# Kernel tuning notes

Measured on AMD Instinct MI355X. Metric: run time of the kernel, lower is better.

## Reference

```python
import jax, jax.numpy as jnp
import numpy as np

N, C, HW, HEADS = 2048, 16, 8, 4
F = C * HW * HW  # 1024
E = 16384
EPS = 1e-5
NEG_SLOPE = 0.2


def _bn(x, g, b):
    # training-mode BatchNorm2d over (N, H, W)
    m = x.mean(axis=(0, 2, 3), keepdims=True)
    v = x.var(axis=(0, 2, 3), keepdims=True)
    return (x - m) * jax.lax.rsqrt(v + EPS) * g[None, :, None, None] + b[None, :, None, None]


def _conv1x1(x, w, b):
    # 1x1 conv == per-pixel linear: w is [out_c, in_c]
    return jnp.einsum('nchw,oc->nohw', x, w) + b[None, :, None, None]


def _gatv2(xf, edge_index, wl, bl, wr, br, att, bias_gat):
    # xf: [N, F] node features
    xl = (xf @ wl + bl).reshape(N, HEADS, F)  # source-side transform (lin_l)
    xr = (xf @ wr + br).reshape(N, HEADS, F)  # target-side transform (lin_r)
    src, dst = edge_index[0], edge_index[1]
    loops = jnp.arange(N)
    # PyG default: remove existing self loops (mask them) then add self loops
    src_f = jnp.concatenate([src, loops])
    dst_f = jnp.concatenate([dst, loops])
    valid = jnp.concatenate([src != dst, jnp.ones((N,), bool)])
    xj = xl[src_f]                                   # [E+N, HEADS, F] gather
    e = jax.nn.leaky_relu(xj + xr[dst_f], negative_slope=NEG_SLOPE)
    logits = jnp.einsum('ehf,hf->eh', e, att)        # [E+N, HEADS]
    logits = jnp.where(valid[:, None], logits, -jnp.inf)
    mx = jax.lax.stop_gradient(jax.ops.segment_max(logits, dst_f, num_segments=N))
    expv = jnp.where(valid[:, None], jnp.exp(logits - mx[dst_f]), 0.0)
    denom = jax.ops.segment_sum(expv, dst_f, num_segments=N)
    alpha = expv / denom[dst_f]                      # segment softmax over incoming edges
    out = jax.ops.segment_sum(alpha[:, :, None] * xj, dst_f, num_segments=N)  # [N, HEADS, F]
    return out.reshape(N, HEADS * F) + bias_gat


def setup_inputs() -> dict:
    key = jax.random.key(0)
    ks = jax.random.split(key, 8)
    s = 0.02
    return {
        'x': jax.random.normal(ks[0], (N, C, HW, HW), jnp.float32),
        'edge_index': jax.random.randint(ks[1], (2, E), 0, N),
        'w1': jax.random.normal(ks[2], (C, C), jnp.float32) * s,
        'b1': jnp.zeros((C,), jnp.float32),
        'g1': jnp.ones((C,), jnp.float32),
        'be1': jnp.zeros((C,), jnp.float32),
        'wl': jax.random.normal(ks[3], (F, HEADS * F), jnp.float32) * s,
        'bl': jnp.zeros((HEADS * F,), jnp.float32),
        'wr': jax.random.normal(ks[4], (F, HEADS * F), jnp.float32) * s,
        'br': jnp.zeros((HEADS * F,), jnp.float32),
        'att': jax.random.normal(ks[5], (HEADS, F), jnp.float32) * s,
        'bias_gat': jnp.zeros((HEADS * F,), jnp.float32),
        'w2': jax.random.normal(ks[6], (C, HEADS * C), jnp.float32) * s,
        'b2': jnp.zeros((C,), jnp.float32),
        'g2': jnp.ones((C,), jnp.float32),
        'be2': jnp.zeros((C,), jnp.float32),
    }


def reference(x, edge_index, w1, b1, g1, be1, wl, bl, wr, br, att, bias_gat, w2, b2, g2, be2):
    res = x
    y = _bn(_conv1x1(x, w1, b1), g1, be1)            # fc1: Conv2d 1x1 + BN
    yf = y.reshape(N, F)
    g = _gatv2(yf, edge_index, wl, bl, wr, br, att, bias_gat)
    g = g.reshape(N, HEADS * C, HW, HW)
    out = _bn(_conv1x1(g, w2, b2), g2, be2)          # fc2: Conv2d 1x1 + BN
    return out + res                                  # DropPath(0.0) == Identity
```

## Files before the change

kernel.cpp:

```cpp
#include <hip/hip_runtime.h>
#include <stdint.h>

#define N_NODES 2048
#define F_DIM   1024
#define HEADS   4
#define NF      4096
#define ROW     8192
#define E_EDGES 16384
#define MAXE    (E_EDGES + N_NODES)
#define BN_EPS  1e-5f
#define NSLOPE  0.2f

typedef unsigned short ushort_t;
typedef __attribute__((ext_vector_type(8))) short bf16x8;
typedef __attribute__((ext_vector_type(4))) float f32x4;
typedef __attribute__((ext_vector_type(8))) unsigned short us8;

__device__ __forceinline__ float b2f(unsigned short u) {
    union { unsigned int i; float f; } x; x.i = ((unsigned int)u) << 16; return x.f;
}
__device__ __forceinline__ unsigned short f2b(float f) {
    union { float f; unsigned int i; } x; x.f = f;
    unsigned int r = x.i + 0x7fffu + ((x.i >> 16) & 1u);
    return (unsigned short)(r >> 16);
}
__device__ __forceinline__ ushort_t ld_canon(const void* src, size_t i, int f32) {
    return f32 ? f2b(((const float*)src)[i]) : ((const ushort_t*)src)[i];
}
__device__ __forceinline__ float ld_f(const void* src, size_t i, int f32) {
    return f32 ? ((const float*)src)[i] : b2f(((const ushort_t*)src)[i]);
}

__device__ __forceinline__ int sniff_f32_blk(const ushort_t* xu, int* lds_flag) {
    int t = threadIdx.x;
    if (t < 64) {
        unsigned e = (xu[2 * t] >> 7) & 0xFF;
        unsigned long long m = __ballot(e >= 0x90u);
        if (t == 0) *lds_flag = (__popcll(m) >= 3) ? 1 : 0;
    }
    __syncthreads();
    return *lds_flag;
}
__device__ __forceinline__ int sniff_i64_blk(const int* ei_raw, int* lds_flag) {
    int t = threadIdx.x;
    if (t < 64) {
        unsigned long long m = __ballot(ei_raw[2 * t + 1] != 0);
        if (t == 0) *lds_flag = (m == 0ull) ? 1 : 0;
    }
    __syncthreads();
    return *lds_flag;
}

__global__ __launch_bounds__(256) void k_prep(
    const void* __restrict__ wl, const void* __restrict__ wr,
    const int* __restrict__ ei_raw, const ushort_t* __restrict__ xu,
    ushort_t* __restrict__ wT, int* __restrict__ counts)
{
    __shared__ ushort_t tl[64][65];
    __shared__ int sfl;
    int b = blockIdx.x, t = threadIdx.x;
    if (b < 2048) {
        int f32 = sniff_f32_blk(xu, &sfl);
        int z = b >> 10, rem = b & 1023;
        int bx = (rem & 63) * 64, by = (rem >> 6) * 64;
        const void* in = z ? wr : wl;
        ushort_t* outT = wT + (size_t)z * 4194304ull;
        #pragma unroll
        for (int i = 0; i < 16; ++i) {
            int idx = t + i * 256;
            int r = idx >> 6, c = idx & 63;
            tl[r][c] = ld_canon(in, (size_t)(by + r) * 4096 + bx + c, f32);
        }
        __syncthreads();
        #pragma unroll
        for (int i = 0; i < 16; ++i) {
            int idx = t + i * 256;
            int r = idx >> 6, c = idx & 63;
            outT[(size_t)(bx + r) * 1024 + by + c] = tl[c][r];
        }
    } else {
        int i64 = sniff_i64_blk(ei_raw, &sfl);
        int idx = (b - 2048) * 256 + t;
        if (idx < E_EDGES) {
            int s = i64 ? ei_raw[2 * idx] : ei_raw[idx];
            int d = i64 ? ei_raw[2 * (E_EDGES + idx)] : ei_raw[E_EDGES + idx];
            if (s != d) atomicAdd(&counts[d], 1);
        } else if (idx < MAXE) {
            atomicAdd(&counts[idx - E_EDGES], 1);
        }
    }
}

__global__ __launch_bounds__(256) void k_fc1(
    const void* __restrict__ x, const void* __restrict__ w1, const void* __restrict__ b1,
    ushort_t* __restrict__ y0b, float* __restrict__ ps, float* __restrict__ pq)
{
    __shared__ float xs[1024];
    __shared__ float sw[256];
    __shared__ float sb[16];
    __shared__ int sfl;
    int f32 = sniff_f32_blk((const ushort_t*)x, &sfl);
    int tid = threadIdx.x;
    sw[tid] = ld_f(w1, tid, f32);
    if (tid < 16) sb[tid] = ld_f(b1, tid, f32);
    int wave = tid >> 6, lane = tid & 63;
    float s[4] = {0,0,0,0}, q[4] = {0,0,0,0};
    for (int nn = 0; nn < 8; ++nn) {
        int n = blockIdx.x * 8 + nn;
        __syncthreads();
        #pragma unroll
        for (int i = 0; i < 4; ++i) {
            int idx = tid + i * 256;
            xs[idx] = ld_f(x, (size_t)n * 1024 + idx, f32);
        }
        __syncthreads();
        #pragma unroll
        for (int i = 0; i < 4; ++i) {
            int o = wave * 4 + i;
            float acc = sb[o];
            #pragma unroll
            for (int c = 0; c < 16; ++c) acc += xs[c * 64 + lane] * sw[o * 16 + c];
            y0b[(size_t)n * 1024 + o * 64 + lane] = f2b(acc);
            s[i] += acc; q[i] += acc * acc;
        }
    }
    #pragma unroll
    for (int i = 0; i < 4; ++i)
        for (int mm = 1; mm < 64; mm <<= 1) {
            s[i] += __shfl_xor(s[i], mm);
            q[i] += __shfl_xor(q[i], mm);
        }
    if (lane == 0)
        #pragma unroll
        for (int i = 0; i < 4; ++i) {
            ps[blockIdx.x * 16 + wave * 4 + i] = s[i];
            pq[blockIdx.x * 16 + wave * 4 + i] = q[i];
        }
}

__global__ __launch_bounds__(256) void k_mid(
    const int* __restrict__ ei_raw, const int* __restrict__ counts,
    int* __restrict__ cursor, int* __restrict__ offs, int* __restrict__ esrc,
    const float* __restrict__ ps, const float* __restrict__ pq,
    const void* __restrict__ g1, const void* __restrict__ be1,
    const ushort_t* __restrict__ xu, float* __restrict__ ss)
{
    __shared__ int offl[2048];
    __shared__ int ts[256];
    __shared__ int sfl;
    __shared__ float rs[16][16], rq[16][16];
    int t = threadIdx.x;
    if (blockIdx.x < 72) {
        int i64 = sniff_i64_blk(ei_raw, &sfl);
        int loc[8]; int tot = 0;
        #pragma unroll
        for (int j = 0; j < 8; ++j) { loc[j] = counts[t * 8 + j]; tot += loc[j]; }
        ts[t] = tot; __syncthreads();
        for (int s = 1; s < 256; s <<= 1) {
            int v = (t >= s) ? ts[t - s] : 0;
            __syncthreads();
            ts[t] += v;
            __syncthreads();
        }
        int run = ts[t] - tot;
        #pragma unroll
        for (int j = 0; j < 8; ++j) { offl[t * 8 + j] = run; run += loc[j]; }
        __syncthreads();
        if (blockIdx.x == 0) {
            #pragma unroll
            for (int j = 0; j < 8; ++j) offs[t * 8 + j] = offl[t * 8 + j];
            if (t == 255) offs[2048] = run;
        }
        int idx = blockIdx.x * 256 + t;
        if (idx < E_EDGES) {
            int s = i64 ? ei_raw[2 * idx] : ei_raw[idx];
            int d = i64 ? ei_raw[2 * (E_EDGES + idx)] : ei_raw[E_EDGES + idx];
            if (s != d) esrc[offl[d] + atomicAdd(&cursor[d], 1)] = s;
        } else if (idx < MAXE) {
            int n = idx - E_EDGES;
            esrc[offl[n] + atomicAdd(&cursor[n], 1)] = n;
        }
    } else {
        int f32 = sniff_f32_blk(xu, &sfl);
        int ch = t & 15, seg = t >> 4;
        float s = 0.f, q = 0.f;
        for (int j = 0; j < 16; ++j) {
            int b = seg * 16 + j;
            s += ps[b * 16 + ch]; q += pq[b * 16 + ch];
        }
        rs[seg][ch] = s; rq[seg][ch] = q;
        __syncthreads();
        if (t < 16) {
            float S = 0.f, Q = 0.f;
            #pragma unroll
            for (int g = 0; g < 16; ++g) { S += rs[g][t]; Q += rq[g][t]; }
            const float inv = 1.0f / 131072.0f;
            float mean = S * inv;
            float var  = Q * inv - mean * mean;
            float sc = ld_f(g1, t, f32) * rsqrtf(var + BN_EPS);
            ss[t] = sc;
            ss[16 + t] = ld_f(be1, t, f32) - mean * sc;
        }
    }
}

__global__ __launch_bounds__(256) void k_norm(
    const ushort_t* __restrict__ y0b, const float* __restrict__ ss,
    ushort_t* __restrict__ xf)
{
    __shared__ float scs[16], shs[16];
    int t = threadIdx.x;
    if (t < 16) { scs[t] = ss[t]; shs[t] = ss[16 + t]; }
    __syncthreads();
    size_t base = (size_t)blockIdx.x * 4096 + t * 16;
    int ch = ((int)(base >> 6)) & 15;
    float sc = scs[ch], sh = shs[ch];
    us8 v0 = *(const us8*)(y0b + base), v1 = *(const us8*)(y0b + base + 8);
    us8 o0, o1;
    #pragma unroll
    for (int j = 0; j < 8; ++j) {
        o0[j] = f2b(b2f(v0[j]) * sc + sh);
        o1[j] = f2b(b2f(v1[j]) * sc + sh);
    }
    *(us8*)(xf + base) = o0;
    *(us8*)(xf + base + 8) = o1;
}

__global__ __launch_bounds__(256) void k_gemm(
    const ushort_t* __restrict__ A, const ushort_t* __restrict__ BT,
    const void* __restrict__ blr, const void* __restrict__ brr,
    const ushort_t* __restrict__ xu, ushort_t* __restrict__ out)
{
    __shared__ __align__(16) ushort_t smem[16384];
    ushort_t* As0 = smem;
    ushort_t* As1 = smem + 4096;
    ushort_t* Bs0 = smem + 8192;
    ushort_t* Bs1 = smem + 12288;
    ushort_t* cs  = smem;
    __shared__ int sfl;
    int f32 = sniff_f32_blk(xu, &sfl);
    int tid = threadIdx.x;
    int wv = tid >> 6, ln = tid & 63;
    int m0 = blockIdx.y * 128, n0 = blockIdx.x * 128;
    int wm = (wv >> 1) * 64, wn = (wv & 1) * 64;
    int lr = ln & 15, quad = ln >> 4;

    f32x4 acc[4][4];
    #pragma unroll
    for (int i = 0; i < 4; ++i)
        #pragma unroll
        for (int j = 0; j < 4; ++j) acc[i][j] = (f32x4){0.f, 0.f, 0.f, 0.f};

    for (int k0 = 0; k0 < 1024; k0 += 64) {
        #pragma unroll
        for (int i = 0; i < 2; ++i) {
            int cbase = i * 256 + wv * 64;
            int ci = cbase + ln;
            int m = ci >> 2, kc = ci & 3;
            const ushort_t* ga = A + (size_t)(m0 + m) * 1024 + k0 + kc * 8;
            __builtin_amdgcn_global_load_lds(
                (const __attribute__((address_space(1))) void*)ga,
                (__attribute__((address_space(3))) void*)(&As0[cbase * 8]), 16, 0, 0);
            __builtin_amdgcn_global_load_lds(
                (const __attribute__((address_space(1))) void*)(ga + 32),
                (__attribute__((address_space(3))) void*)(&As1[cbase * 8]), 16, 0, 0);
            const ushort_t* gb = BT + (size_t)(n0 + m) * 1024 + k0 + kc * 8;
            __builtin_amdgcn_global_load_lds(
                (const __attribute__((address_space(1))) void*)gb,
                (__attribute__((address_space(3))) void*)(&Bs0[cbase * 8]), 16, 0, 0);
            __builtin_amdgcn_global_load_lds(
                (const __attribute__((address_space(1))) void*)(gb + 32),
                (__attribute__((address_space(3))) void*)(&Bs1[cbase * 8]), 16, 0, 0);
        }
        __syncthreads();
        #pragma unroll
        for (int p = 0; p < 2; ++p) {
            const ushort_t* Ap = p ? As1 : As0;
            const ushort_t* Bp = p ? Bs1 : Bs0;
            bf16x8 af[4], bfr[4];
            #pragma unroll
            for (int i = 0; i < 4; ++i)
                af[i] = *(const bf16x8*)(&Ap[(wm + i * 16 + lr) * 32 + quad * 8]);
            #pragma unroll
            for (int j = 0; j < 4; ++j)
                bfr[j] = *(const bf16x8*)(&Bp[(wn + j * 16 + lr) * 32 + quad * 8]);
            #pragma unroll
            for (int i = 0; i < 4; ++i)
                #pragma unroll
                for (int j = 0; j < 4; ++j)
                    acc[i][j] = __builtin_amdgcn_mfma_f32_16x16x32_bf16(af[i], bfr[j], acc[i][j], 0, 0, 0);
        }
        __syncthreads();
    }
    float bj[4];
    #pragma unroll
    for (int j = 0; j < 4; ++j) {
        int colg = n0 + wn + j * 16 + lr;
        bj[j] = (colg < 4096) ? ld_f(blr, colg, f32) : ld_f(brr, colg - 4096, f32);
    }
    #pragma unroll
    for (int ph = 0; ph < 2; ++ph) {
        if ((wv >> 1) == ph) {
            #pragma unroll
            for (int i = 0; i < 4; ++i)
                #pragma unroll
                for (int j = 0; j < 4; ++j) {
                    int col = wn + j * 16 + lr;
                    #pragma unroll
                    for (int r = 0; r < 4; ++r)
                        cs[(i * 16 + quad * 4 + r) * 136 + col] = f2b(acc[i][j][r] + bj[j]);
                }
        }
        __syncthreads();
        #pragma unroll
        for (int rr = 0; rr < 4; ++rr) {
            int slot = rr * 256 + tid;
            int row = slot >> 4, seg = slot & 15;
            us8 v = *(const us8*)&cs[row * 136 + seg * 8];
            *(us8*)(out + (size_t)(m0 + ph * 64 + row) * ROW + n0 + seg * 8) = v;
        }
        __syncthreads();
    }
}

__global__ __launch_bounds__(64) void k_gat(
    const ushort_t* __restrict__ xlr,
    const void* __restrict__ att, const void* __restrict__ bg,
    const ushort_t* __restrict__ xu,
    const int* __restrict__ offsets, const int* __restrict__ esrc,
    ushort_t* __restrict__ g)
{
    int bx = blockIdx.x;
    int d = bx >> 2, h = bx & 3;
    int l = threadIdx.x;
    int f32;
    {
        unsigned e = (xu[2 * l] >> 7) & 0xFF;
        unsigned long long m = __ballot(e >= 0x90u);
        f32 = (__popcll(m) >= 3) ? 1 : 0;
    }
    int off = offsets[d], deg = offsets[d + 1] - off;
    size_t hF = (size_t)h * F_DIM + l * 16;

    float xrv[16], attv[16];
    {
        const ushort_t* xp = xlr + ((size_t)d * ROW + NF + hF);
        us8 x0 = *(const us8*)xp, x1 = *(const us8*)(xp + 8);
        #pragma unroll
        for (int j = 0; j < 8; ++j) {
            xrv[j] = b2f(x0[j]); xrv[8 + j] = b2f(x1[j]);
            attv[j]     = ld_f(att, hF + j, f32);
            attv[8 + j] = ld_f(att, hF + 8 + j, f32);
        }
    }
    float acc[16];
    #pragma unroll
    for (int j = 0; j < 16; ++j) acc[j] = 0.f;
    float s_run = 0.f;

    for (int c0 = 0; c0 < deg; c0 += 64) {
        int cnt = min(64, deg - c0);
        int eidx = esrc[off + c0 + (l < cnt ? l : 0)];
        int e = 0;
        for (; e + 3 < cnt; e += 4) {
            int i0 = __shfl(eidx, e),     i1 = __shfl(eidx, e + 1);
            int i2 = __shfl(eidx, e + 2), i3 = __shfl(eidx, e + 3);
            const ushort_t* p0 = xlr + ((size_t)i0 * ROW + hF);
            const ushort_t* p1 = xlr + ((size_t)i1 * ROW + hF);
            const ushort_t* p2 = xlr + ((size_t)i2 * ROW + hF);
            const ushort_t* p3 = xlr + ((size_t)i3 * ROW + hF);
            us8 v0[4], v1[4];
            v0[0] = *(const us8*)p0; v1[0] = *(const us8*)(p0 + 8);
            v0[1] = *(const us8*)p1; v1[1] = *(const us8*)(p1 + 8);
            v0[2] = *(const us8*)p2; v1[2] = *(const us8*)(p2 + 8);
            v0[3] = *(const us8*)p3; v1[3] = *(const us8*)(p3 + 8);
            float tt[4];
            #pragma unroll
            for (int k = 0; k < 4; ++k) {
                float t0 = 0.f;
                #pragma unroll
                for (int j = 0; j < 8; ++j) {
                    float u;
                    u = b2f(v0[k][j]) + xrv[j];     u = u > 0.f ? u : NSLOPE * u; t0 += u * attv[j];
                    u = b2f(v1[k][j]) + xrv[8 + j]; u = u > 0.f ? u : NSLOPE * u; t0 += u * attv[8 + j];
                }
                tt[k] = t0;
            }
            #pragma unroll
            for (int mm = 1; mm < 64; mm <<= 1) {
                tt[0] += __shfl_xor(tt[0], mm);
                tt[1] += __shfl_xor(tt[1], mm);
                tt[2] += __shfl_xor(tt[2], mm);
                tt[3] += __shfl_xor(tt[3], mm);
            }
            float w0 = __expf(tt[0]), w1 = __expf(tt[1]);
            float w2v = __expf(tt[2]), w3 = __expf(tt[3]);
            s_run += w0 + w1 + w2v + w3;
            #pragma unroll
            for (int j = 0; j < 8; ++j) {
                acc[j]     += w0 * b2f(v0[0][j]) + w1 * b2f(v0[1][j])
                            + w2v * b2f(v0[2][j]) + w3 * b2f(v0[3][j]);
                acc[8 + j] += w0 * b2f(v1[0][j]) + w1 * b2f(v1[1][j])
                            + w2v * b2f(v1[2][j]) + w3 * b2f(v1[3][j]);
            }
        }
        for (; e < cnt; ++e) {
            int i0 = __shfl(eidx, e);
            const ushort_t* p = xlr + ((size_t)i0 * ROW + hF);
            us8 a0 = *(const us8*)p, a1 = *(const us8*)(p + 8);
            float t0 = 0.f;
            #pragma unroll
            for (int j = 0; j < 8; ++j) {
                float u;
                u = b2f(a0[j]) + xrv[j];     u = u > 0.f ? u : NSLOPE * u; t0 += u * attv[j];
                u = b2f(a1[j]) + xrv[8 + j]; u = u > 0.f ? u : NSLOPE * u; t0 += u * attv[8 + j];
            }
            #pragma unroll
            for (int mm = 1; mm < 64; mm <<= 1) t0 += __shfl_xor(t0, mm);
            float w0 = __expf(t0);
            s_run += w0;
            #pragma unroll
            for (int j = 0; j < 8; ++j) {
                acc[j]     += w0 * b2f(a0[j]);
                acc[8 + j] += w0 * b2f(a1[j]);
            }
        }
    }
    float inv = 1.0f / s_run;
    ushort_t* gp = g + ((size_t)d * NF + hF);
    us8 outv0, outv1;
    #pragma unroll
    for (int j = 0; j < 8; ++j) {
        outv0[j] = f2b(acc[j] * inv + ld_f(bg, hF + j, f32));
        outv1[j] = f2b(acc[8 + j] * inv + ld_f(bg, hF + 8 + j, f32));
    }
    *(us8*)gp = outv0;
    *(us8*)(gp + 8) = outv1;
}

__global__ __launch_bounds__(256) void k_fc2(
    const ushort_t* __restrict__ g, const void* __restrict__ w2, const void* __restrict__ b2,
    const ushort_t* __restrict__ xu,
    ushort_t* __restrict__ zb, float* __restrict__ ps, float* __restrict__ pq)
{
    __shared__ float gs[4096];
    __shared__ float sw[1024];
    __shared__ float sb[16];
    __shared__ int sfl;
    int f32 = sniff_f32_blk(xu, &sfl);
    int tid = threadIdx.x;
    #pragma unroll
    for (int i = 0; i < 4; ++i) sw[tid + i * 256] = ld_f(w2, tid + i * 256, f32);
    if (tid < 16) sb[tid] = ld_f(b2, tid, f32);
    int wave = tid >> 6, lane = tid & 63;
    float s[4] = {0,0,0,0}, q[4] = {0,0,0,0};
    for (int nn = 0; nn < 8; ++nn) {
        int n = blockIdx.x * 8 + nn;
        __syncthreads();
        {
            const ushort_t* gp = g + (size_t)n * 4096 + tid * 16;
            us8 v0 = *(const us8*)gp, v1 = *(const us8*)(gp + 8);
            #pragma unroll
            for (int j = 0; j < 8; ++j) {
                gs[tid * 16 + j] = b2f(v0[j]);
                gs[tid * 16 + 8 + j] = b2f(v1[j]);
            }
        }
        __syncthreads();
        #pragma unroll
        for (int i = 0; i < 4; ++i) {
            int o = wave * 4 + i;
            float acc = sb[o];
            #pragma unroll
            for (int k = 0; k < 64; ++k) acc += gs[k * 64 + lane] * sw[o * 64 + k];
            zb[(size_t)n * 1024 + o * 64 + lane] = f2b(acc);
            s[i] += acc; q[i] += acc * acc;
        }
    }
    #pragma unroll
    for (int i = 0; i < 4; ++i)
        for (int mm = 1; mm < 64; mm <<= 1) {
            s[i] += __shfl_xor(s[i], mm);
            q[i] += __shfl_xor(q[i], mm);
        }
    if (lane == 0)
        #pragma unroll
        for (int i = 0; i < 4; ++i) {
            ps[blockIdx.x * 16 + wave * 4 + i] = s[i];
            pq[blockIdx.x * 16 + wave * 4 + i] = q[i];
        }
}

__global__ __launch_bounds__(256) void k_out(
    const ushort_t* __restrict__ zb, const void* __restrict__ x,
    const float* __restrict__ ps, const float* __restrict__ pq,
    const void* __restrict__ g2, const void* __restrict__ be2,
    void* __restrict__ out)
{
    __shared__ float red[2][64];
    __shared__ float scs[16], shs[16];
    __shared__ int sfl;
    int f32 = sniff_f32_blk((const ushort_t*)x, &sfl);
    int t = threadIdx.x, lane = t & 63, wv = t >> 6;
    float s = 0.f, q = 0.f;
    #pragma unroll
    for (int i = 0; i < 16; ++i) { s += ps[i * 256 + t]; q += pq[i * 256 + t]; }
    s += __shfl_xor(s, 16); q += __shfl_xor(q, 16);
    s += __shfl_xor(s, 32); q += __shfl_xor(q, 32);
    if (lane < 16) { red[0][wv * 16 + lane] = s; red[1][wv * 16 + lane] = q; }
    __syncthreads();
    if (t < 16) {
        float S = red[0][t] + red[0][16 + t] + red[0][32 + t] + red[0][48 + t];
        float Q = red[1][t] + red[1][16 + t] + red[1][32 + t] + red[1][48 + t];
        const float inv = 1.0f / 131072.0f;
        float mean = S * inv;
        float var  = Q * inv - mean * mean;
        float sc = ld_f(g2, t, f32) * rsqrtf(var + BN_EPS);
        scs[t] = sc;
        shs[t] = ld_f(be2, t, f32) - mean * sc;
    }
    __syncthreads();
    size_t base = (size_t)blockIdx.x * 8192;
    #pragma unroll
    for (int i = 0; i < 32; ++i) {
        size_t k = base + t + i * 256;
        int ch = ((int)k >> 6) & 15;
        float val = b2f(zb[k]) * scs[ch] + shs[ch] + ld_f(x, k, f32);
        if (f32) ((float*)out)[k] = val;
        else     ((ushort_t*)out)[k] = f2b(val);
    }
}

extern "C" void kernel_launch(void* const* d_in, const int* in_sizes, int n_in,
                              void* d_out, int out_size, void* d_ws, size_t ws_size,
                              hipStream_t stream)
{
    const void* x   = d_in[0];
    const void* ei  = d_in[1];
    const void* w1  = d_in[2];
    const void* b1  = d_in[3];
    const void* g1  = d_in[4];
    const void* be1 = d_in[5];
    const void* wl  = d_in[6];
    const void* bl  = d_in[7];
    const void* wr  = d_in[8];
    const void* br  = d_in[9];
    const void* att = d_in[10];
    const void* bg  = d_in[11];
    const void* w2  = d_in[12];
    const void* b2  = d_in[13];
    const void* g2  = d_in[14];
    const void* be2 = d_in[15];
    (void)in_sizes; (void)n_in; (void)out_size; (void)ws_size;

    char* wsb = (char*)d_ws;
    size_t o = 0;
    auto alloc = [&](size_t bytes) -> void* {
        void* p = wsb + o;
        o = (o + bytes + 255) & ~(size_t)255;
        return p;
    };
    float*    ss    = (float*)alloc(32 * 4);
    ushort_t* y0b   = (ushort_t*)alloc(2097152ull * 2);
    ushort_t* xf    = (ushort_t*)alloc(2097152ull * 2);
    ushort_t* zb    = (ushort_t*)alloc(2097152ull * 2);
    ushort_t* wT    = (ushort_t*)alloc(8388608ull * 2);
    ushort_t* gbuf  = wT;
    ushort_t* xlr   = (ushort_t*)alloc(16777216ull * 2);
    float* p1s = (float*)alloc(256 * 16 * 4);
    float* p1q = (float*)alloc(256 * 16 * 4);
    float* p2s = (float*)alloc(256 * 16 * 4);
    float* p2q = (float*)alloc(256 * 16 * 4);
    int* counts = (int*)alloc(2048 * 4);
    int* cursor = (int*)alloc(2048 * 4);
    int* offs   = (int*)alloc(2049 * 4);
    int* esrc   = (int*)alloc(MAXE * 4);

    hipMemsetAsync(counts, 0, 2 * 2048 * 4, stream);
    k_prep<<<2120, 256, 0, stream>>>(wl, wr, (const int*)ei, (const ushort_t*)x, wT, counts);
    k_fc1<<<256, 256, 0, stream>>>(x, w1, b1, y0b, p1s, p1q);
    k_mid<<<73, 256, 0, stream>>>((const int*)ei, counts, cursor, offs, esrc,
                                  p1s, p1q, g1, be1, (const ushort_t*)x, ss);
    k_norm<<<512, 256, 0, stream>>>(y0b, ss, xf);
    k_gemm<<<dim3(64, 16), 256, 0, stream>>>(xf, wT, bl, br, (const ushort_t*)x, xlr);
    k_gat<<<N_NODES * HEADS, 64, 0, stream>>>(xlr, att, bg, (const ushort_t*)x, offs, esrc, gbuf);
    k_fc2<<<256, 256, 0, stream>>>(gbuf, w2, b2, (const ushort_t*)x, zb, p2s, p2q);
    k_out<<<256, 256, 0, stream>>>(zb, x, p2s, p2q, g2, be2, d_out);
}
```

Before: 275.6 us.

## Derive fc1 BN stats from input covariance and fuse normalize into conv

Computes BatchNorm statistics for the first 1x1 conv analytically from per-channel input means and the 16x16 input covariance. This lets the conv, scale and shift be folded into a single kernel that writes the normalized bf16 features directly, so the intermediate y0b buffer and the separate normalize pass go away. The price is a second read of x and a reduction over a larger partial-covariance buffer in a single block. It also remaps GEMM block indices so that blocks on the same XCD share N tiles, aiming for better L2 reuse.

```diff
diff --git a/kernel.cpp b/kernel.cpp
--- a/kernel.cpp
+++ b/kernel.cpp
@@ -91,64 +91,49 @@
     }
 }
 
-__global__ __launch_bounds__(256) void k_fc1(
-    const void* __restrict__ x, const void* __restrict__ w1, const void* __restrict__ b1,
-    ushort_t* __restrict__ y0b, float* __restrict__ ps, float* __restrict__ pq)
-{
-    __shared__ float xs[1024];
-    __shared__ float sw[256];
-    __shared__ float sb[16];
+__global__ __launch_bounds__(256) void k_stats(
+    const void* __restrict__ x, const ushort_t* __restrict__ xu,
+    float* __restrict__ psum, float* __restrict__ pcov)
+{
+    __shared__ float xs[16 * 65];
     __shared__ int sfl;
-    int f32 = sniff_f32_blk((const ushort_t*)x, &sfl);
-    int tid = threadIdx.x;
-    sw[tid] = ld_f(w1, tid, f32);
-    if (tid < 16) sb[tid] = ld_f(b1, tid, f32);
-    int wave = tid >> 6, lane = tid & 63;
-    float s[4] = {0,0,0,0}, q[4] = {0,0,0,0};
+    int f32 = sniff_f32_blk(xu, &sfl);
+    int t = threadIdx.x;
+    int c1 = t >> 4, c2 = t & 15;
+    float cov = 0.f, s = 0.f;
     for (int nn = 0; nn < 8; ++nn) {
         int n = blockIdx.x * 8 + nn;
         __syncthreads();
         #pragma unroll
         for (int i = 0; i < 4; ++i) {
-            int idx = tid + i * 256;
-            xs[idx] = ld_f(x, (size_t)n * 1024 + idx, f32);
-        }
-        __syncthreads();
-        #pragma unroll
-        for (int i = 0; i < 4; ++i) {
-            int o = wave * 4 + i;
-            float acc = sb[o];
-            #pragma unroll
-            for (int c = 0; c < 16; ++c) acc += xs[c * 64 + lane] * sw[o * 16 + c];
-            y0b[(size_t)n * 1024 + o * 64 + lane] = f2b(acc);
-            s[i] += acc; q[i] += acc * acc;
-        }
-    }
-    #pragma unroll
-    for (int i = 0; i < 4; ++i)
-        for (int mm = 1; mm < 64; mm <<= 1) {
-            s[i] += __shfl_xor(s[i], mm);
-            q[i] += __shfl_xor(q[i], mm);
-        }
-    if (lane == 0)
-        #pragma unroll
-        for (int i = 0; i < 4; ++i) {
-            ps[blockIdx.x * 16 + wave * 4 + i] = s[i];
-            pq[blockIdx.x * 16 + wave * 4 + i] = q[i];
-        }
+            int idx = t + i * 256;
+            int c = idx >> 6, p = idx & 63;
+            xs[c * 65 + p] = ld_f(x, (size_t)n * 1024 + idx, f32);
+        }
+        __syncthreads();
+        #pragma unroll
+        for (int p = 0; p < 64; ++p)
+            cov += xs[c1 * 65 + p] * xs[c2 * 65 + p];
+        if (t < 16) {
+            #pragma unroll
+            for (int p = 0; p < 64; ++p) s += xs[t * 65 + p];
+        }
+    }
+    pcov[blockIdx.x * 256 + t] = cov;
+    if (t < 16) psum[blockIdx.x * 16 + t] = s;
 }
 
 __global__ __launch_bounds__(256) void k_mid(
     const int* __restrict__ ei_raw, const int* __restrict__ counts,
     int* __restrict__ cursor, int* __restrict__ offs, int* __restrict__ esrc,
-    const float* __restrict__ ps, const float* __restrict__ pq,
+    const float* __restrict__ psum, const float* __restrict__ pcov,
+    const void* __restrict__ w1, const void* __restrict__ b1,
     const void* __restrict__ g1, const void* __restrict__ be1,
     const ushort_t* __restrict__ xu, float* __restrict__ ss)
 {
     __shared__ int offl[2048];
     __shared__ int ts[256];
     __shared__ int sfl;
-    __shared__ float rs[16][16], rq[16][16];
     int t = threadIdx.x;
     if (blockIdx.x < 72) {
         int i64 = sniff_i64_blk(ei_raw, &sfl);
@@ -181,22 +166,30 @@
             esrc[offl[n] + atomicAdd(&cursor[n], 1)] = n;
         }
     } else {
+        __shared__ float covr[256];
+        __shared__ float mu[16];
+        __shared__ float wsh[256];
         int f32 = sniff_f32_blk(xu, &sfl);
-        int ch = t & 15, seg = t >> 4;
-        float s = 0.f, q = 0.f;
-        for (int j = 0; j < 16; ++j) {
-            int b = seg * 16 + j;
-            s += ps[b * 16 + ch]; q += pq[b * 16 + ch];
-        }
-        rs[seg][ch] = s; rq[seg][ch] = q;
-        __syncthreads();
+        float c = 0.f;
+        for (int b = 0; b < 256; ++b) c += pcov[b * 256 + t];
+        covr[t] = c;
+        wsh[t] = ld_f(w1, t, f32);
         if (t < 16) {
-            float S = 0.f, Q = 0.f;
-            #pragma unroll
-            for (int g = 0; g < 16; ++g) { S += rs[g][t]; Q += rq[g][t]; }
+            float s = 0.f;
+            for (int b = 0; b < 256; ++b) s += psum[b * 16 + t];
+            mu[t] = s * (1.0f / 131072.0f);
+        }
+        __syncthreads();
+        if (t < 16) {
             const float inv = 1.0f / 131072.0f;
-            float mean = S * inv;
-            float var  = Q * inv - mean * mean;
+            float mean = ld_f(b1, t, f32);
+            float var = 0.f;
+            for (int ca = 0; ca < 16; ++ca) {
+                float wa = wsh[t * 16 + ca];
+                mean += wa * mu[ca];
+                for (int cb = 0; cb < 16; ++cb)
+                    var += wa * wsh[t * 16 + cb] * (covr[ca * 16 + cb] * inv - mu[ca] * mu[cb]);
+            }
             float sc = ld_f(g1, t, f32) * rsqrtf(var + BN_EPS);
             ss[t] = sc;
             ss[16 + t] = ld_f(be1, t, f32) - mean * sc;
@@ -204,26 +197,41 @@
     }
 }
 
-__global__ __launch_bounds__(256) void k_norm(
-    const ushort_t* __restrict__ y0b, const float* __restrict__ ss,
-    ushort_t* __restrict__ xf)
-{
+__global__ __launch_bounds__(256) void k_fc1n(
+    const void* __restrict__ x, const void* __restrict__ w1, const void* __restrict__ b1,
+    const float* __restrict__ ss, ushort_t* __restrict__ xf)
+{
+    __shared__ float xs[1024];
+    __shared__ float sw[256];
+    __shared__ float sb[16];
     __shared__ float scs[16], shs[16];
-    int t = threadIdx.x;
-    if (t < 16) { scs[t] = ss[t]; shs[t] = ss[16 + t]; }
+    __shared__ int sfl;
+    int f32 = sniff_f32_blk((const ushort_t*)x, &sfl);
+    int tid = threadIdx.x;
+    float wraw = ld_f(w1, tid, f32);
+    if (tid < 16) { scs[tid] = ss[tid]; shs[tid] = ss[16 + tid]; }
     __syncthreads();
-    size_t base = (size_t)blockIdx.x * 4096 + t * 16;
-    int ch = ((int)(base >> 6)) & 15;
-    float sc = scs[ch], sh = shs[ch];
-    us8 v0 = *(const us8*)(y0b + base), v1 = *(const us8*)(y0b + base + 8);
-    us8 o0, o1;
-    #pragma unroll
-    for (int j = 0; j < 8; ++j) {
-        o0[j] = f2b(b2f(v0[j]) * sc + sh);
-        o1[j] = f2b(b2f(v1[j]) * sc + sh);
-    }
-    *(us8*)(xf + base) = o0;
-    *(us8*)(xf + base + 8) = o1;
+    sw[tid] = wraw * scs[tid >> 4];
+    if (tid < 16) sb[tid] = scs[tid] * ld_f(b1, tid, f32) + shs[tid];
+    int wave = tid >> 6, lane = tid & 63;
+    for (int nn = 0; nn < 8; ++nn) {
+        int n = blockIdx.x * 8 + nn;
+        __syncthreads();
+        #pragma unroll
+        for (int i = 0; i < 4; ++i) {
+            int idx = tid + i * 256;
+            xs[idx] = ld_f(x, (size_t)n * 1024 + idx, f32);
+        }
+        __syncthreads();
+        #pragma unroll
+        for (int i = 0; i < 4; ++i) {
+            int o = wave * 4 + i;
+            float acc = sb[o];
+            #pragma unroll
+            for (int c = 0; c < 16; ++c) acc += xs[c * 64 + lane] * sw[o * 16 + c];
+            xf[(size_t)n * 1024 + o * 64 + lane] = f2b(acc);
+        }
+    }
 }
 
 __global__ __launch_bounds__(256) void k_gemm(
@@ -241,7 +249,12 @@
     int f32 = sniff_f32_blk(xu, &sfl);
     int tid = threadIdx.x;
     int wv = tid >> 6, ln = tid & 63;
-    int m0 = blockIdx.y * 128, n0 = blockIdx.x * 128;
+    int lin = blockIdx.x + gridDim.x * blockIdx.y;
+    int xcd = lin & 7;
+    int j = lin >> 3;
+    int nt = xcd * 8 + (j & 7);
+    int mt = j >> 3;
+    int m0 = mt * 128, n0 = nt * 128;
     int wm = (wv >> 1) * 64, wn = (wv & 1) * 64;
     int lr = ln & 15, quad = ln >> 4;
 
@@ -249,7 +262,7 @@
     #pragma unroll
     for (int i = 0; i < 4; ++i)
         #pragma unroll
-        for (int j = 0; j < 4; ++j) acc[i][j] = (f32x4){0.f, 0.f, 0.f, 0.f};
+        for (int j2 = 0; j2 < 4; ++j2) acc[i][j2] = (f32x4){0.f, 0.f, 0.f, 0.f};
 
     for (int k0 = 0; k0 < 1024; k0 += 64) {
         #pragma unroll
@@ -282,21 +295,21 @@
             for (int i = 0; i < 4; ++i)
                 af[i] = *(const bf16x8*)(&Ap[(wm + i * 16 + lr) * 32 + quad * 8]);
             #pragma unroll
-            for (int j = 0; j < 4; ++j)
-                bfr[j] = *(const bf16x8*)(&Bp[(wn + j * 16 + lr) * 32 + quad * 8]);
+            for (int j2 = 0; j2 < 4; ++j2)
+                bfr[j2] = *(const bf16x8*)(&Bp[(wn + j2 * 16 + lr) * 32 + quad * 8]);
             #pragma unroll
             for (int i = 0; i < 4; ++i)
                 #pragma unroll
-                for (int j = 0; j < 4; ++j)
-                    acc[i][j] = __builtin_amdgcn_mfma_f32_16x16x32_bf16(af[i], bfr[j], acc[i][j], 0, 0, 0);
+                for (int j2 = 0; j2 < 4; ++j2)
+                    acc[i][j2] = __builtin_amdgcn_mfma_f32_16x16x32_bf16(af[i], bfr[j2], acc[i][j2], 0, 0, 0);
         }
         __syncthreads();
     }
     float bj[4];
     #pragma unroll
-    for (int j = 0; j < 4; ++j) {
-        int colg = n0 + wn + j * 16 + lr;
-        bj[j] = (colg < 4096) ? ld_f(blr, colg, f32) : ld_f(brr, colg - 4096, f32);
+    for (int j2 = 0; j2 < 4; ++j2) {
+        int colg = n0 + wn + j2 * 16 + lr;
+        bj[j2] = (colg < 4096) ? ld_f(blr, colg, f32) : ld_f(brr, colg - 4096, f32);
     }
     #pragma unroll
     for (int ph = 0; ph < 2; ++ph) {
@@ -304,11 +317,11 @@
             #pragma unroll
             for (int i = 0; i < 4; ++i)
                 #pragma unroll
-                for (int j = 0; j < 4; ++j) {
-                    int col = wn + j * 16 + lr;
+                for (int j2 = 0; j2 < 4; ++j2) {
+                    int col = wn + j2 * 16 + lr;
                     #pragma unroll
                     for (int r = 0; r < 4; ++r)
-                        cs[(i * 16 + quad * 4 + r) * 136 + col] = f2b(acc[i][j][r] + bj[j]);
+                        cs[(i * 16 + quad * 4 + r) * 136 + col] = f2b(acc[i][j2][r] + bj[j2]);
                 }
         }
         __syncthreads();
@@ -561,16 +574,15 @@
         return p;
     };
     float*    ss    = (float*)alloc(32 * 4);
-    ushort_t* y0b   = (ushort_t*)alloc(2097152ull * 2);
     ushort_t* xf    = (ushort_t*)alloc(2097152ull * 2);
     ushort_t* zb    = (ushort_t*)alloc(2097152ull * 2);
     ushort_t* wT    = (ushort_t*)alloc(8388608ull * 2);
     ushort_t* gbuf  = wT;
     ushort_t* xlr   = (ushort_t*)alloc(16777216ull * 2);
-    float* p1s = (float*)alloc(256 * 16 * 4);
-    float* p1q = (float*)alloc(256 * 16 * 4);
-    float* p2s = (float*)alloc(256 * 16 * 4);
-    float* p2q = (float*)alloc(256 * 16 * 4);
+    float* psum = (float*)alloc(256 * 16 * 4);
+    float* pcov = (float*)alloc(256 * 256 * 4);
+    float* p2s  = (float*)alloc(256 * 16 * 4);
+    float* p2q  = (float*)alloc(256 * 16 * 4);
     int* counts = (int*)alloc(2048 * 4);
     int* cursor = (int*)alloc(2048 * 4);
     int* offs   = (int*)alloc(2049 * 4);
@@ -578,10 +590,10 @@
 
     hipMemsetAsync(counts, 0, 2 * 2048 * 4, stream);
     k_prep<<<2120, 256, 0, stream>>>(wl, wr, (const int*)ei, (const ushort_t*)x, wT, counts);
-    k_fc1<<<256, 256, 0, stream>>>(x, w1, b1, y0b, p1s, p1q);
+    k_stats<<<256, 256, 0, stream>>>(x, (const ushort_t*)x, psum, pcov);
     k_mid<<<73, 256, 0, stream>>>((const int*)ei, counts, cursor, offs, esrc,
-                                  p1s, p1q, g1, be1, (const ushort_t*)x, ss);
-    k_norm<<<512, 256, 0, stream>>>(y0b, ss, xf);
+                                  psum, pcov, w1, b1, g1, be1, (const ushort_t*)x, ss);
+    k_fc1n<<<256, 256, 0, stream>>>(x, w1, b1, ss, xf);
     k_gemm<<<dim3(64, 16), 256, 0, stream>>>(xf, wT, bl, br, (const ushort_t*)x, xlr);
     k_gat<<<N_NODES * HEADS, 64, 0, stream>>>(xlr, att, bg, (const ushort_t*)x, offs, esrc, gbuf);
     k_fc2<<<256, 256, 0, stream>>>(gbuf, w2, b2, (const ushort_t*)x, zb, p2s, p2q);
```

Result: slower. 297.5 us (+8.0%).
